# Kernel optimization log

Hardware: AMD Instinct MI355X
Metric: run time of the kernel (lower is better)

The kernel has to match this reference:

```python
import jax, jax.numpy as jnp
import numpy as np
import math

B, N, J, D, H, LMAX = 2, 512, 32, 256, 8, 2
M = 2 * LMAX + 1  # multiplier = 5
CUTOFF = 5.0
HEAD_DIM_NORM = D  # head_dim arg is None -> self.head_dim = hidden_dim


def _layer_norm(x, w, b):
    mu = jnp.mean(x, axis=-1, keepdims=True)
    var = jnp.mean((x - mu) ** 2, axis=-1, keepdims=True)
    return (x - mu) / jnp.sqrt(var + 1e-5) * w + b


def _gather(x, idx):
    # x: [B, N, ...], idx: [B, N, J] -> [B, N, J, ...]
    return jax.vmap(lambda a, i: a[i])(x, idx)


def setup_inputs() -> dict:
    key = jax.random.key(0)
    ks = jax.random.split(key, 18)
    s = 1.0 / math.sqrt(D)
    inp = {
        "h": jax.random.normal(ks[0], (B, N, D), jnp.float32),
        "X1": jax.random.normal(ks[1], (B, N, 3, D), jnp.float32),
        "X2": jax.random.normal(ks[2], (B, N, 5, D), jnp.float32),
        "r1_ij": jax.random.normal(ks[3], (B, N, J, 3), jnp.float32),
        "r2_ij": jax.random.normal(ks[4], (B, N, J, 5), jnp.float32),
        "t_ij": jax.random.normal(ks[5], (B, N, J, D), jnp.float32),
        "r_ij": jax.random.uniform(ks[6], (B, N, J), jnp.float32) * 6.0,  # some edges beyond cutoff
        "neighbor_index": jax.random.randint(ks[7], (B, N, J), 0, N),
        "neighbor_mask": jax.random.randint(ks[8], (B, N, J), 0, 2).astype(bool),
        "ln_w": jnp.ones((D,), jnp.float32),
        "ln_b": jnp.zeros((D,), jnp.float32),
        "W_q": jax.random.normal(ks[9], (D, D), jnp.float32) * s,
        "W_k": jax.random.normal(ks[10], (D, D), jnp.float32) * s,
        "W_re": jax.random.normal(ks[11], (D, D), jnp.float32) * s,
        "W_rs": jax.random.normal(ks[12], (M * D, D), jnp.float32) * s,
        "gs_w1": jax.random.normal(ks[13], (D, D), jnp.float32) * s,
        "gs_w2": jax.random.normal(ks[14], (M * D, D), jnp.float32) * s,
        "gv_w1": jax.random.normal(ks[15], (D, D), jnp.float32) * s,
        "gv_w2": jax.random.normal(ks[16], (M * D, D), jnp.float32) * s,
    }
    return inp


def reference(h, X1, X2, r1_ij, r2_ij, t_ij, r_ij, neighbor_index, neighbor_mask,
              ln_w, ln_b, W_q, W_k, W_re, W_rs, gs_w1, gs_w2, gv_w1, gv_w2):
    silu = jax.nn.silu
    hn = _layer_norm(h, ln_w, ln_b)
    q = hn @ W_q.T                                   # [B,N,D]
    k = hn @ W_k.T                                   # [B,N,D]
    x = silu(hn @ gs_w1.T) @ gs_w2.T                 # gamma_s -> [B,N,M*D]
    v = silu(hn @ gv_w1.T) @ gv_w2.T                 # gamma_v -> [B,N,M*D]
    t_attn = silu(t_ij @ W_re.T)                     # [B,N,J,D]
    t_filt = t_ij @ W_rs.T                           # [B,N,J,M*D]

    dh = D // H                                      # per-head dim for q/k = 32
    qi = q.reshape(B, N, H, dh)
    kj = _gather(k, neighbor_index).reshape(B, N, J, H, dh)
    vj = _gather(v, neighbor_index).reshape(B, N, J, H, M * dh)
    xj = _gather(x, neighbor_index)                  # [B,N,J,M*D]
    X1j = _gather(X1, neighbor_index)                # [B,N,J,3,D]
    X2j = _gather(X2, neighbor_index)                # [B,N,J,5,D]
    ta = t_attn.reshape(B, N, J, H, dh)

    attn = jnp.einsum('bihd,bijhd,bijhd->bhij', qi, kj, ta)
    attn = jnp.where(neighbor_mask[:, None], attn, -1e9)
    attn = jax.nn.softmax(attn, axis=-1)
    n_edges = neighbor_mask.astype(jnp.float32).sum(-1)          # [B,N]
    norm = jnp.sqrt(n_edges) / math.sqrt(HEAD_DIM_NORM)          # scale_edge=True
    attn = attn * norm[:, None, :, None]

    sea = jnp.einsum('bhij,bijhe->bijhe', attn, vj).reshape(B, N, J, M * D)
    cut = 0.5 * (jnp.cos(r_ij * math.pi / CUTOFF) + 1.0) * (r_ij < CUTOFF).astype(jnp.float32)
    spatial = t_filt * xj * cut[..., None]
    out = (spatial + sea).reshape(B, N, J, M, D)

    o_s = out[..., 0, :]                              # [B,N,J,D]
    o_d1, o_d2 = out[..., 1, :], out[..., 2, :]
    o_t1, o_t2 = out[..., 3, :], out[..., 4, :]

    d_h = o_s.sum(axis=2)                             # [B,N,D]
    dX1 = (r1_ij[..., None] * o_d1[..., None, :] + X1j * o_t1[..., None, :]).sum(axis=2)
    dX2 = (r2_ij[..., None] * o_d2[..., None, :] + X2j * o_t2[..., None, :]).sum(axis=2)
    return d_h, dX1, dX2
```

## Files before the change

### kernel.cpp

```cpp
#include <hip/hip_runtime.h>

#define BB 2
#define NN 512
#define JJ 32
#define DD 256
#define HH 8
#define MM 5
#define MD 1280

#define OFF_WQ   0
#define OFF_WK   65536
#define OFF_GS1  131072
#define OFF_GV1  196608
#define OFF_WRE  262144
#define OFF_GS2  327680
#define OFF_GV2  655360
#define OFF_WRS  983040
#define OFF_Q    1310720
#define OFF_K    1572864
#define OFF_X    1835008
#define OFF_V    3145728
#define OFF_MSK  4456448
#define OFF_ATTN 4464640

__device__ __forceinline__ float silu_f(float x){ return x / (1.0f + expf(-x)); }

__global__ void mask_norm_kernel(const unsigned int* __restrict__ raw,
                                 unsigned char* __restrict__ outm) {
    __shared__ int flag_s;
    const int tid = threadIdx.x;
    const int blk = blockIdx.x;
    if (tid == 0) flag_s = 0;
    __syncthreads();
    int bad = 0;
    for (int i = tid; i < 1024; i += 256) bad |= (raw[blk*1024 + i] > 1u) ? 1 : 0;
    if (bad) atomicOr(&flag_s, 1);
    __syncthreads();
    const int base = blk * 4096;
    if (flag_s) {
        const unsigned char* rb = (const unsigned char*)raw;
        for (int i = tid; i < 4096; i += 256) outm[base + i] = rb[base + i] ? 1 : 0;
    } else {
        for (int i = tid; i < 4096; i += 256) outm[base + i] = raw[base + i] ? 1 : 0;
    }
}

__global__ __launch_bounds__(256) void transpose_kernel(
        const float* __restrict__ Wq, const float* __restrict__ Wk,
        const float* __restrict__ gs1, const float* __restrict__ gv1,
        const float* __restrict__ Wre, const float* __restrict__ gs2,
        const float* __restrict__ gv2, const float* __restrict__ Wrs,
        float* __restrict__ ws) {
    __shared__ float tile[32][33];
    const int bid = blockIdx.x;
    const float* src; float* dst; int R, tr, tc;
    if (bid < 320) {
        int m = bid >> 6, t = bid & 63;
        tr = t >> 3; tc = t & 7; R = 256;
        src = (m==0)?Wq:(m==1)?Wk:(m==2)?gs1:(m==3)?gv1:Wre;
        dst = ws + m*65536;
    } else {
        int b2 = bid - 320;
        int m = b2 / 320, t = b2 % 320;
        tr = t >> 3; tc = t & 7; R = 1280;
        src = (m==0)?gs2:(m==1)?gv2:Wrs;
        dst = ws + OFF_GS2 + m*327680;
    }
    const int r = threadIdx.x >> 5, c = threadIdx.x & 31;
    #pragma unroll
    for (int s = 0; s < 4; s++)
        tile[r + 8*s][c] = src[(size_t)(tr*32 + r + 8*s)*256 + tc*32 + c];
    __syncthreads();
    #pragma unroll
    for (int s = 0; s < 4; s++)
        dst[(size_t)(tc*32 + r + 8*s)*R + tr*32 + c] = tile[c][r + 8*s];
}

__global__ __launch_bounds__(256) void node_kernel(const float* __restrict__ h,
                                                   const float* __restrict__ ln_w,
                                                   const float* __restrict__ ln_b,
                                                   float* __restrict__ ws) {
    __shared__ float hs[4][256];
    __shared__ float s1s[4][256];
    __shared__ float v1s[4][256];
    __shared__ float mu_s[4], rstd_s[4];
    const int tid = threadIdx.x;
    const int row0 = blockIdx.x * 4;

    #pragma unroll
    for (int r = 0; r < 4; r++) hs[r][tid] = h[(size_t)(row0 + r)*256 + tid];
    __syncthreads();

    {
        int g = tid >> 6, l = tid & 63;
        float s = 0.f;
        #pragma unroll
        for (int k = 0; k < 4; k++) s += hs[g][l + 64*k];
        #pragma unroll
        for (int off = 32; off > 0; off >>= 1) s += __shfl_xor(s, off, 64);
        float mu = s * (1.0f/256.0f);
        float v = 0.f;
        #pragma unroll
        for (int k = 0; k < 4; k++) { float d0 = hs[g][l + 64*k] - mu; v += d0*d0; }
        #pragma unroll
        for (int off = 32; off > 0; off >>= 1) v += __shfl_xor(v, off, 64);
        if (l == 0) { mu_s[g] = mu; rstd_s[g] = rsqrtf(v*(1.0f/256.0f) + 1e-5f); }
    }
    __syncthreads();
    {
        float w = ln_w[tid], bb = ln_b[tid];
        #pragma unroll
        for (int r = 0; r < 4; r++) hs[r][tid] = (hs[r][tid] - mu_s[r]) * rstd_s[r] * w + bb;
    }
    __syncthreads();

    {
        float aq[4], ak[4], a1[4], a2[4];
        #pragma unroll
        for (int r = 0; r < 4; r++) { aq[r]=0.f; ak[r]=0.f; a1[r]=0.f; a2[r]=0.f; }
        const float* WqT  = ws + OFF_WQ;
        const float* WkT  = ws + OFF_WK;
        const float* G1T  = ws + OFF_GS1;
        const float* Gv1T = ws + OFF_GV1;
        for (int e = 0; e < 256; e++) {
            float wq = WqT[e*256 + tid];
            float wk = WkT[e*256 + tid];
            float w1 = G1T[e*256 + tid];
            float w2 = Gv1T[e*256 + tid];
            #pragma unroll
            for (int r = 0; r < 4; r++) {
                float hv = hs[r][e];
                aq[r] += hv*wq; ak[r] += hv*wk; a1[r] += hv*w1; a2[r] += hv*w2;
            }
        }
        #pragma unroll
        for (int r = 0; r < 4; r++) {
            ws[OFF_Q + (size_t)(row0 + r)*256 + tid] = aq[r];
            ws[OFF_K + (size_t)(row0 + r)*256 + tid] = ak[r];
            s1s[r][tid] = silu_f(a1[r]);
            v1s[r][tid] = silu_f(a2[r]);
        }
    }
    __syncthreads();

    {
        float ax[4][5], av[4][5];
        #pragma unroll
        for (int r = 0; r < 4; r++)
            #pragma unroll
            for (int m = 0; m < 5; m++) { ax[r][m]=0.f; av[r][m]=0.f; }
        const float* G2T  = ws + OFF_GS2;
        const float* Gv2T = ws + OFF_GV2;
        for (int e = 0; e < 256; e++) {
            float wx[5], wv[5];
            #pragma unroll
            for (int m = 0; m < 5; m++) {
                wx[m] = G2T [e*1280 + m*256 + tid];
                wv[m] = Gv2T[e*1280 + m*256 + tid];
            }
            #pragma unroll
            for (int r = 0; r < 4; r++) {
                float s1v = s1s[r][e], v1v = v1s[r][e];
                #pragma unroll
                for (int m = 0; m < 5; m++) { ax[r][m] += s1v*wx[m]; av[r][m] += v1v*wv[m]; }
            }
        }
        #pragma unroll
        for (int r = 0; r < 4; r++)
            #pragma unroll
            for (int m = 0; m < 5; m++) {
                ws[OFF_X + (size_t)(row0 + r)*1280 + m*256 + tid] = ax[r][m];
                ws[OFF_V + (size_t)(row0 + r)*1280 + m*256 + tid] = av[r][m];
            }
    }
}

__global__ __launch_bounds__(256) void attn_kernel(const float* __restrict__ t_ij,
                                                   const int* __restrict__ nbr,
                                                   float* __restrict__ ws) {
    __shared__ float t_s[JJ][DD];
    __shared__ float q_s[DD];
    __shared__ float attn_s[JJ][HH];
    __shared__ int   nbr_s[JJ];
    __shared__ int   msk_s[JJ];
    __shared__ float norm_s;

    const int tid = threadIdx.x;
    const int bi  = blockIdx.x;
    const int b   = bi >> 9;
    const unsigned char* mask = (const unsigned char*)(ws + OFF_MSK);

    if (tid < JJ) {
        nbr_s[tid] = nbr[bi*JJ + tid];
        msk_s[tid] = mask[bi*JJ + tid] ? 1 : 0;
    }
    q_s[tid] = ws[OFF_Q + (size_t)bi*256 + tid];
    for (int j = 0; j < JJ; j++)
        t_s[j][tid] = t_ij[((size_t)bi*JJ + j)*256 + tid];
    __syncthreads();
    if (tid == 0) {
        int n = 0;
        for (int j = 0; j < JJ; j++) n += msk_s[j];
        norm_s = sqrtf((float)n) * (1.0f/16.0f);
    }

    float ta[JJ];
    #pragma unroll
    for (int j = 0; j < JJ; j++) ta[j] = 0.f;
    {
        const float* WreT = ws + OFF_WRE;
        for (int e = 0; e < 256; e += 4) {
            float w4[4];
            #pragma unroll
            for (int s = 0; s < 4; s++) w4[s] = WreT[(e+s)*256 + tid];
            #pragma unroll
            for (int j = 0; j < JJ; j++) {
                const float4 tv = *reinterpret_cast<const float4*>(&t_s[j][e]);
                ta[j] += tv.x*w4[0] + tv.y*w4[1] + tv.z*w4[2] + tv.w*w4[3];
            }
        }
    }
    {
        float qv = q_s[tid];
        #pragma unroll
        for (int j = 0; j < JJ; j++) {
            float kv = ws[OFF_K + (size_t)(b*NN + nbr_s[j])*256 + tid];
            float p = qv * kv * silu_f(ta[j]);
            #pragma unroll
            for (int off = 16; off > 0; off >>= 1) p += __shfl_xor(p, off, 32);
            if ((tid & 31) == 0) attn_s[j][tid >> 5] = p;
        }
    }
    __syncthreads();
    {
        int hh = tid >> 5, j = tid & 31;
        float l = msk_s[j] ? attn_s[j][hh] : -1e9f;
        float mx = l;
        #pragma unroll
        for (int off = 16; off > 0; off >>= 1) mx = fmaxf(mx, __shfl_xor(mx, off, 32));
        float e0 = expf(l - mx);
        float ssum = e0;
        #pragma unroll
        for (int off = 16; off > 0; off >>= 1) ssum += __shfl_xor(ssum, off, 32);
        ws[OFF_ATTN + (size_t)bi*256 + j*8 + hh] = (e0 / ssum) * norm_s;
    }
}

template<int G>
__global__ __launch_bounds__(256, 3) void combine_kernel(
        const float* __restrict__ t_ij, const float* __restrict__ r_ij,
        const int* __restrict__ nbr,
        const float* __restrict__ r1, const float* __restrict__ r2,
        const float* __restrict__ X1, const float* __restrict__ X2,
        const float* __restrict__ ws, float* __restrict__ out) {
    __shared__ float t_s[JJ][DD];
    __shared__ float attn_l[JJ][HH];
    __shared__ float cut_s[JJ];
    __shared__ float r1_s[JJ][3];
    __shared__ float r2_s[JJ][5];
    __shared__ int   nbr_s[JJ];

    const int tid = threadIdx.x;
    const int bi  = blockIdx.x;
    const int b   = bi >> 9;

    if (tid < JJ) {
        int eidx = bi*JJ + tid;
        nbr_s[tid] = nbr[eidx];
        float r = r_ij[eidx];
        cut_s[tid] = (r < 5.0f) ? 0.5f*(cosf(r * 0.62831853071795864f) + 1.0f) : 0.0f;
        #pragma unroll
        for (int c = 0; c < 3; c++) r1_s[tid][c] = r1[eidx*3 + c];
        #pragma unroll
        for (int c = 0; c < 5; c++) r2_s[tid][c] = r2[eidx*5 + c];
    }
    attn_l[tid >> 3][tid & 7] = ws[OFF_ATTN + (size_t)bi*256 + tid];
    for (int j = 0; j < JJ; j++)
        t_s[j][tid] = t_ij[((size_t)bi*JJ + j)*256 + tid];
    __syncthreads();

    constexpr int m0 = (G == 0) ? 0 : (G == 1) ? 1 : 2;
    constexpr int m1 = m0 + 2;

    float tf0[JJ];
    float tf1[JJ];
    #pragma unroll
    for (int j = 0; j < JJ; j++) { tf0[j] = 0.f; if (G > 0) tf1[j] = 0.f; }
    {
        const float* W0 = ws + OFF_WRS + m0*256 + tid;
        const float* W1 = ws + OFF_WRS + m1*256 + tid;
        for (int e = 0; e < 256; e += 4) {
            float wa[4], wb[4];
            #pragma unroll
            for (int s = 0; s < 4; s++) wa[s] = W0[(size_t)(e+s)*1280];
            if (G > 0) {
                #pragma unroll
                for (int s = 0; s < 4; s++) wb[s] = W1[(size_t)(e+s)*1280];
            }
            #pragma unroll
            for (int j = 0; j < JJ; j++) {
                const float4 tv = *reinterpret_cast<const float4*>(&t_s[j][e]);
                tf0[j] += tv.x*wa[0] + tv.y*wa[1] + tv.z*wa[2] + tv.w*wa[3];
                if (G > 0)
                    tf1[j] += tv.x*wb[0] + tv.y*wb[1] + tv.z*wb[2] + tv.w*wb[3];
            }
        }
    }

    const float* Xb = ws + OFF_X + (size_t)b*NN*1280;
    const float* Vb = ws + OFF_V + (size_t)b*NN*1280;
    const int h0 = (m0*256 + tid) / 160;
    const int h1 = (m1*256 + tid) / 160;
    float acc[5] = {0.f, 0.f, 0.f, 0.f, 0.f};

    #pragma unroll
    for (int j = 0; j < JJ; j++) {
        const int nb = nbr_s[j];
        const float cut = cut_s[j];
        const float* xr = Xb + (size_t)nb*1280;
        const float* vr = Vb + (size_t)nb*1280;
        float o0 = tf0[j]*xr[m0*256 + tid]*cut + attn_l[j][h0]*vr[m0*256 + tid];
        if (G == 0) {
            acc[0] += o0;
        } else {
            float o1 = tf1[j]*xr[m1*256 + tid]*cut + attn_l[j][h1]*vr[m1*256 + tid];
            if (G == 1) {
                const float* x1r = X1 + ((size_t)(b*NN + nb))*768;
                acc[0] += r1_s[j][0]*o0 + x1r[tid]*o1;
                acc[1] += r1_s[j][1]*o0 + x1r[256 + tid]*o1;
                acc[2] += r1_s[j][2]*o0 + x1r[512 + tid]*o1;
            } else {
                const float* x2r = X2 + ((size_t)(b*NN + nb))*1280;
                #pragma unroll
                for (int c = 0; c < 5; c++)
                    acc[c] += r2_s[j][c]*o0 + x2r[c*256 + tid]*o1;
            }
        }
    }

    if (G == 0) {
        out[(size_t)bi*256 + tid] = acc[0];
    } else if (G == 1) {
        #pragma unroll
        for (int c = 0; c < 3; c++)
            out[262144 + ((size_t)bi*3 + c)*256 + tid] = acc[c];
    } else {
        #pragma unroll
        for (int c = 0; c < 5; c++)
            out[1048576 + ((size_t)bi*5 + c)*256 + tid] = acc[c];
    }
}

extern "C" void kernel_launch(void* const* d_in, const int* in_sizes, int n_in,
                              void* d_out, int out_size, void* d_ws, size_t ws_size,
                              hipStream_t stream) {
    const float* h    = (const float*)d_in[0];
    const float* X1   = (const float*)d_in[1];
    const float* X2   = (const float*)d_in[2];
    const float* r1   = (const float*)d_in[3];
    const float* r2   = (const float*)d_in[4];
    const float* t_ij = (const float*)d_in[5];
    const float* r_ij = (const float*)d_in[6];
    const int*   nbr  = (const int*)d_in[7];
    const unsigned int* mask_raw = (const unsigned int*)d_in[8];
    const float* ln_w = (const float*)d_in[9];
    const float* ln_b = (const float*)d_in[10];
    const float* Wq   = (const float*)d_in[11];
    const float* Wk   = (const float*)d_in[12];
    const float* Wre  = (const float*)d_in[13];
    const float* Wrs  = (const float*)d_in[14];
    const float* gs1  = (const float*)d_in[15];
    const float* gs2  = (const float*)d_in[16];
    const float* gv1  = (const float*)d_in[17];
    const float* gv2  = (const float*)d_in[18];

    float* ws  = (float*)d_ws;
    float* out = (float*)d_out;

    hipLaunchKernelGGL(mask_norm_kernel, dim3(8), dim3(256), 0, stream,
                       mask_raw, (unsigned char*)(ws + OFF_MSK));
    hipLaunchKernelGGL(transpose_kernel, dim3(1280), dim3(256), 0, stream,
                       Wq, Wk, gs1, gv1, Wre, gs2, gv2, Wrs, ws);
    hipLaunchKernelGGL(node_kernel, dim3(BB*NN/4), dim3(256), 0, stream,
                       h, ln_w, ln_b, ws);
    hipLaunchKernelGGL(attn_kernel, dim3(BB*NN), dim3(256), 0, stream,
                       t_ij, nbr, ws);
    hipLaunchKernelGGL((combine_kernel<0>), dim3(BB*NN), dim3(256), 0, stream,
                       t_ij, r_ij, nbr, r1, r2, X1, X2, ws, out);
    hipLaunchKernelGGL((combine_kernel<1>), dim3(BB*NN), dim3(256), 0, stream,
                       t_ij, r_ij, nbr, r1, r2, X1, X2, ws, out);
    hipLaunchKernelGGL((combine_kernel<2>), dim3(BB*NN), dim3(256), 0, stream,
                       t_ij, r_ij, nbr, r1, r2, X1, X2, ws, out);
}
```

Baseline: 811.2 us.

## Fuse three combine kernels into one, tiling neighbors in groups of eight

The three templated combine kernels are merged into a single kernel that computes all five filter components per thread. The t_ij tile is loaded into shared memory once instead of three times, and each W_rs load is reused across five outputs. Neighbors are processed in chunks of 8 so the 40 per-chunk accumulators fit in registers. Launch bounds are raised to 4 waves per SIMD, which may cause register spills, and each block now does more serial work with less parallelism across launches.

```diff
diff --git a/kernel.cpp b/kernel.cpp
--- a/kernel.cpp
+++ b/kernel.cpp
@@ -246,8 +246,7 @@
     }
 }
 
-template<int G>
-__global__ __launch_bounds__(256, 3) void combine_kernel(
+__global__ __launch_bounds__(256, 4) void combine_all_kernel(
         const float* __restrict__ t_ij, const float* __restrict__ r_ij,
         const int* __restrict__ nbr,
         const float* __restrict__ r1, const float* __restrict__ r2,
@@ -279,76 +278,75 @@
         t_s[j][tid] = t_ij[((size_t)bi*JJ + j)*256 + tid];
     __syncthreads();
 
-    constexpr int m0 = (G == 0) ? 0 : (G == 1) ? 1 : 2;
-    constexpr int m1 = m0 + 2;
-
-    float tf0[JJ];
-    float tf1[JJ];
-    #pragma unroll
-    for (int j = 0; j < JJ; j++) { tf0[j] = 0.f; if (G > 0) tf1[j] = 0.f; }
-    {
-        const float* W0 = ws + OFF_WRS + m0*256 + tid;
-        const float* W1 = ws + OFF_WRS + m1*256 + tid;
-        for (int e = 0; e < 256; e += 4) {
-            float wa[4], wb[4];
-            #pragma unroll
-            for (int s = 0; s < 4; s++) wa[s] = W0[(size_t)(e+s)*1280];
-            if (G > 0) {
-                #pragma unroll
-                for (int s = 0; s < 4; s++) wb[s] = W1[(size_t)(e+s)*1280];
-            }
-            #pragma unroll
-            for (int j = 0; j < JJ; j++) {
-                const float4 tv = *reinterpret_cast<const float4*>(&t_s[j][e]);
-                tf0[j] += tv.x*wa[0] + tv.y*wa[1] + tv.z*wa[2] + tv.w*wa[3];
-                if (G > 0)
-                    tf1[j] += tv.x*wb[0] + tv.y*wb[1] + tv.z*wb[2] + tv.w*wb[3];
-            }
-        }
-    }
-
+    int hm[5];
+    #pragma unroll
+    for (int m = 0; m < 5; m++) hm[m] = (m*256 + tid) / 160;
+
+    const float* WrsT = ws + OFF_WRS;
     const float* Xb = ws + OFF_X + (size_t)b*NN*1280;
     const float* Vb = ws + OFF_V + (size_t)b*NN*1280;
-    const int h0 = (m0*256 + tid) / 160;
-    const int h1 = (m1*256 + tid) / 160;
-    float acc[5] = {0.f, 0.f, 0.f, 0.f, 0.f};
-
-    #pragma unroll
-    for (int j = 0; j < JJ; j++) {
-        const int nb = nbr_s[j];
-        const float cut = cut_s[j];
-        const float* xr = Xb + (size_t)nb*1280;
-        const float* vr = Vb + (size_t)nb*1280;
-        float o0 = tf0[j]*xr[m0*256 + tid]*cut + attn_l[j][h0]*vr[m0*256 + tid];
-        if (G == 0) {
-            acc[0] += o0;
-        } else {
-            float o1 = tf1[j]*xr[m1*256 + tid]*cut + attn_l[j][h1]*vr[m1*256 + tid];
-            if (G == 1) {
-                const float* x1r = X1 + ((size_t)(b*NN + nb))*768;
-                acc[0] += r1_s[j][0]*o0 + x1r[tid]*o1;
-                acc[1] += r1_s[j][1]*o0 + x1r[256 + tid]*o1;
-                acc[2] += r1_s[j][2]*o0 + x1r[512 + tid]*o1;
-            } else {
-                const float* x2r = X2 + ((size_t)(b*NN + nb))*1280;
+
+    float acc_dh = 0.f;
+    float acc1[3] = {0.f, 0.f, 0.f};
+    float acc2[5] = {0.f, 0.f, 0.f, 0.f, 0.f};
+
+    for (int p = 0; p < 4; p++) {
+        const int j0 = p * 8;
+        float tf[8][5];
+        #pragma unroll
+        for (int jj = 0; jj < 8; jj++)
+            #pragma unroll
+            for (int m = 0; m < 5; m++) tf[jj][m] = 0.f;
+
+        for (int e = 0; e < 256; e += 4) {
+            float w[4][5];
+            #pragma unroll
+            for (int s = 0; s < 4; s++)
                 #pragma unroll
-                for (int c = 0; c < 5; c++)
-                    acc[c] += r2_s[j][c]*o0 + x2r[c*256 + tid]*o1;
-            }
-        }
-    }
-
-    if (G == 0) {
-        out[(size_t)bi*256 + tid] = acc[0];
-    } else if (G == 1) {
-        #pragma unroll
-        for (int c = 0; c < 3; c++)
-            out[262144 + ((size_t)bi*3 + c)*256 + tid] = acc[c];
-    } else {
-        #pragma unroll
-        for (int c = 0; c < 5; c++)
-            out[1048576 + ((size_t)bi*5 + c)*256 + tid] = acc[c];
-    }
+                for (int m = 0; m < 5; m++)
+                    w[s][m] = WrsT[(size_t)(e+s)*1280 + m*256 + tid];
+            #pragma unroll
+            for (int jj = 0; jj < 8; jj++) {
+                const float4 tv = *reinterpret_cast<const float4*>(&t_s[j0 + jj][e]);
+                #pragma unroll
+                for (int m = 0; m < 5; m++)
+                    tf[jj][m] += tv.x*w[0][m] + tv.y*w[1][m] + tv.z*w[2][m] + tv.w*w[3][m];
+            }
+        }
+
+        #pragma unroll
+        for (int jj = 0; jj < 8; jj++) {
+            const int j = j0 + jj;
+            const int nb = nbr_s[j];
+            const float cut = cut_s[j];
+            const float* xr  = Xb + (size_t)nb*1280;
+            const float* vr  = Vb + (size_t)nb*1280;
+            const float* x1r = X1 + ((size_t)(b*NN + nb))*768;
+            const float* x2r = X2 + ((size_t)(b*NN + nb))*1280;
+
+            float o0 = tf[jj][0]*xr[0*256 + tid]*cut + attn_l[j][hm[0]]*vr[0*256 + tid];
+            float o1 = tf[jj][1]*xr[1*256 + tid]*cut + attn_l[j][hm[1]]*vr[1*256 + tid];
+            float o2 = tf[jj][2]*xr[2*256 + tid]*cut + attn_l[j][hm[2]]*vr[2*256 + tid];
+            float o3 = tf[jj][3]*xr[3*256 + tid]*cut + attn_l[j][hm[3]]*vr[3*256 + tid];
+            float o4 = tf[jj][4]*xr[4*256 + tid]*cut + attn_l[j][hm[4]]*vr[4*256 + tid];
+
+            acc_dh += o0;
+            #pragma unroll
+            for (int c = 0; c < 3; c++)
+                acc1[c] += r1_s[j][c]*o1 + x1r[c*256 + tid]*o3;
+            #pragma unroll
+            for (int c = 0; c < 5; c++)
+                acc2[c] += r2_s[j][c]*o2 + x2r[c*256 + tid]*o4;
+        }
+    }
+
+    out[(size_t)bi*256 + tid] = acc_dh;
+    #pragma unroll
+    for (int c = 0; c < 3; c++)
+        out[262144 + ((size_t)bi*3 + c)*256 + tid] = acc1[c];
+    #pragma unroll
+    for (int c = 0; c < 5; c++)
+        out[1048576 + ((size_t)bi*5 + c)*256 + tid] = acc2[c];
 }
 
 extern "C" void kernel_launch(void* const* d_in, const int* in_sizes, int n_in,
@@ -385,10 +383,6 @@
                        h, ln_w, ln_b, ws);
     hipLaunchKernelGGL(attn_kernel, dim3(BB*NN), dim3(256), 0, stream,
                        t_ij, nbr, ws);
-    hipLaunchKernelGGL((combine_kernel<0>), dim3(BB*NN), dim3(256), 0, stream,
+    hipLaunchKernelGGL(combine_all_kernel, dim3(BB*NN), dim3(256), 0, stream,
                        t_ij, r_ij, nbr, r1, r2, X1, X2, ws, out);
-    hipLaunchKernelGGL((combine_kernel<1>), dim3(BB*NN), dim3(256), 0, stream,
-                       t_ij, r_ij, nbr, r1, r2, X1, X2, ws, out);
-    hipLaunchKernelGGL((combine_kernel<2>), dim3(BB*NN), dim3(256), 0, stream,
-                       t_ij, r_ij, nbr, r1, r2, X1, X2, ws, out);
-}
+}
```

New measurement: 782.6 us. 1.04x faster.
